# Performance work log

Hardware: AMD Instinct MI355X
Metric: run time of the kernel (lower is better)

## Reference

```python
import jax, jax.numpy as jnp
import numpy as np

N_QUBITS = 12
N_LAYERS = 4
BATCH = 256

# State is kept as shape (batch, 2, 2, ..., 2) with qubit q on axis q+1.
# Z(0) measures the first qubit axis.

def _apply_1q(psi, q, U):
    """Apply a shared 2x2 gate U to qubit q."""
    p = jnp.moveaxis(psi, q + 1, -1)
    p = jnp.einsum('ij,...j->...i', U.astype(psi.dtype), p)
    return jnp.moveaxis(p, -1, q + 1)


def _rz_batch(psi, q, theta):
    """RZ with per-sample angle theta of shape (batch,). RZ = diag(e^{-i t/2}, e^{i t/2})."""
    half = 0.5 * theta
    ph = jnp.stack([jnp.exp(-1j * half), jnp.exp(1j * half)], axis=-1)  # (b, 2)
    ph = ph.reshape((theta.shape[0],) + (1,) * (N_QUBITS - 1) + (2,)).astype(psi.dtype)
    p = jnp.moveaxis(psi, q + 1, -1)
    return jnp.moveaxis(p * ph, -1, q + 1)


def _rz_shared(psi, q, theta):
    """RZ with a scalar (weight) angle shared across the batch."""
    half = 0.5 * theta
    ph = jnp.stack([jnp.exp(-1j * half), jnp.exp(1j * half)]).astype(psi.dtype)  # (2,)
    p = jnp.moveaxis(psi, q + 1, -1)
    return jnp.moveaxis(p * ph, -1, q + 1)


def _ry(psi, q, theta):
    """RY(theta) = [[cos(t/2), -sin(t/2)], [sin(t/2), cos(t/2)]], scalar angle."""
    c, s = jnp.cos(0.5 * theta), jnp.sin(0.5 * theta)
    U = jnp.stack([jnp.stack([c, -s]), jnp.stack([s, c])])
    return _apply_1q(psi, q, U)


def _cx(psi, c, t):
    """CNOT with control c, target t: flip target where control == 1."""
    p = jnp.moveaxis(psi, (c + 1, t + 1), (-2, -1))
    p = jnp.stack([p[..., 0, :], p[..., 1, ::-1]], axis=-2)
    return jnp.moveaxis(p, (-2, -1), (c + 1, t + 1))


def _forward(x, weights):
    b = x.shape[0]
    # H on every qubit starting from |0...0> -> uniform superposition.
    psi = jnp.full((b,) + (2,) * N_QUBITS, np.float32(2.0 ** (-N_QUBITS / 2.0)),
                   dtype=jnp.complex64)
    w = weights.reshape(N_LAYERS, N_QUBITS, 2)  # (layer, qubit, [ry, rz])
    for l in range(N_LAYERS):
        for q in range(N_QUBITS):                 # data re-uploading encoding
            psi = _rz_batch(psi, q, x[:, q])
        for q in range(N_QUBITS):                 # trainable rotations
            psi = _ry(psi, q, w[l, q, 0])
            psi = _rz_shared(psi, q, w[l, q, 1])
        for q in range(N_QUBITS - 1):             # entangling ladder
            psi = _cx(psi, q, q + 1)
    # <Z(0)> = P(qubit0 = 0) - P(qubit0 = 1)
    pr = jnp.sum(jnp.abs(psi) ** 2, axis=tuple(range(2, N_QUBITS + 1)))  # (b, 2)
    return (pr[:, 0] - pr[:, 1])[:, None]  # (b, 1) float32


def setup_inputs() -> dict:
    key = jax.random.key(0)
    kx, kw = jax.random.split(key)
    x = jax.random.normal(kx, (BATCH, N_QUBITS), dtype=jnp.float32)
    weights = jax.random.uniform(kw, (2 * N_LAYERS * N_QUBITS,),
                                 dtype=jnp.float32) * np.float32(2.0 * np.pi)
    return {"x": x, "weights": weights}


def reference(x, weights):
    return _forward(x, weights)
```

## Files before the change

### kernel.cpp

```cpp
#include <hip/hip_runtime.h>

#define NQ 12
#define NL 4
#define DIM 4096
#define BLOCK 512
#define PER_T 8
#define BATCH 256


__device__ __forceinline__ float2 cmul(float2 a, float2 b) {
    return make_float2(a.x * b.x - a.y * b.y, a.x * b.y + a.y * b.x);
}
__device__ __forceinline__ float2 cconj(float2 a) { return make_float2(a.x, -a.y); }

__device__ __forceinline__ float2 fsincos(float ang) {
    float r = ang * 0.15915494309189535f;
    r = r - floorf(r);
    return make_float2(__builtin_amdgcn_cosf(r), __builtin_amdgcn_sinf(r));
}

template <int CTRL>
__device__ __forceinline__ float dppx(float v) {
    int i = __builtin_bit_cast(int, v);
    int r = __builtin_amdgcn_update_dpp(0, i, CTRL, 0xF, 0xF, true);
    return __builtin_bit_cast(float, r);
}
template <int MSK, int CTRL>
__device__ __forceinline__ void ry_dpp(float2* psi, int lane, float c, float s) {
    const float se = (lane & MSK) ? s : -s;
#pragma unroll
    for (int k = 0; k < PER_T; ++k) {
        float px = dppx<CTRL>(psi[k].x);
        float py = dppx<CTRL>(psi[k].y);
        psi[k].x = c * psi[k].x + se * px;
        psi[k].y = c * psi[k].y + se * py;
    }
}
template <int MSK>
__device__ __forceinline__ void ry_shfl(float2* psi, int lane, float c, float s) {
    const float se = (lane & MSK) ? s : -s;
#pragma unroll
    for (int k = 0; k < PER_T; ++k) {
        float px = __shfl_xor(psi[k].x, MSK, 64);
        float py = __shfl_xor(psi[k].y, MSK, 64);
        psi[k].x = c * psi[k].x + se * px;
        psi[k].y = c * psi[k].y + se * py;
    }
}

__global__ __launch_bounds__(BLOCK, 2) void qcp_kernel(
    const float* __restrict__ x,
    const float* __restrict__ w,
    float* __restrict__ out)
{
    __shared__ float2 sP[DIM];
    __shared__ float2 sQ[DIM];
    __shared__ float2 trig[NL * NQ * 2];
    __shared__ float  zhalf[NL * NQ];
    __shared__ float  rbuf[8];

    const int b    = blockIdx.x;
    const int t    = threadIdx.x;
    const int lane = t & 63;
    const int wv   = t >> 6;

    if (t < NL * NQ * 2) trig[t] = fsincos(0.5f * w[t]);
    if (t < NL * NQ) zhalf[t] = 0.5f * w[2 * t + 1];

    float xr[NQ];
#pragma unroll
    for (int q = 0; q < NQ; ++q) xr[q] = x[b * NQ + q];

    int iA[PER_T], iB[PER_T], gI[PER_T];
#pragma unroll
    for (int k = 0; k < PER_T; ++k) {
        iA[k] = lane | (k << 6) | (wv << 9);
        iB[k] = lane | (wv << 6) | (k << 9);
        gI[k] = iA[k] ^ (iA[k] >> 1);
    }

    float2 eph[PER_T];
#pragma unroll
    for (int k = 0; k < PER_T; ++k) {
        int j = iA[k];
        float ang = 0.0f;
#pragma unroll
        for (int q = 0; q < NQ; ++q)
            ang += ((j >> (NQ - 1 - q)) & 1) ? 0.5f * xr[q] : -0.5f * xr[q];
        eph[k] = fsincos(ang);
    }

    float2 psi[PER_T];
#pragma unroll
    for (int k = 0; k < PER_T; ++k) psi[k] = make_float2(0.015625f, 0.0f);

    __syncthreads();

    for (int l = 0; l < NL; ++l) {
        float2 tRY[9];
        float2 tRY0[3], tZ0[3];
        float  zh[6];
        float2 z3, z4, z5;
#pragma unroll
        for (int q = 3; q <= 11; ++q) tRY[q - 3] = trig[(l * NQ + q) * 2];
#pragma unroll
        for (int q = 0; q < 3; ++q) {
            tRY0[q] = trig[(l * NQ + q) * 2 + 0];
            tZ0[q]  = trig[(l * NQ + q) * 2 + 1];
        }
        z3 = trig[(l * NQ + 3) * 2 + 1];
        z4 = trig[(l * NQ + 4) * 2 + 1];
        z5 = trig[(l * NQ + 5) * 2 + 1];
#pragma unroll
        for (int q = 6; q <= 11; ++q) zh[q - 6] = zhalf[l * NQ + q];

#pragma unroll
        for (int k = 0; k < PER_T; ++k) psi[k] = cmul(psi[k], eph[k]);

#pragma unroll
        for (int q = 3; q <= 5; ++q) {
            const int kb = (11 - q) - 6;
            float c = tRY[q - 3].x, s = tRY[q - 3].y;
#pragma unroll
            for (int m = 0; m < PER_T / 2; ++m) {
                int k0 = ((m >> kb) << (kb + 1)) | (m & ((1 << kb) - 1));
                int k1 = k0 | (1 << kb);
                float2 a0 = psi[k0], a1 = psi[k1];
                psi[k0] = make_float2(c * a0.x - s * a1.x, c * a0.y - s * a1.y);
                psi[k1] = make_float2(s * a0.x + c * a1.x, s * a0.y + c * a1.y);
            }
        }

        ry_shfl<32>(psi, lane, tRY[3].x, tRY[3].y);
        ry_shfl<16>(psi, lane, tRY[4].x, tRY[4].y);
        ry_dpp<8, 0x128>(psi, lane, tRY[5].x, tRY[5].y);
        ry_shfl<4>(psi, lane, tRY[6].x, tRY[6].y);
        ry_dpp<2, 0x4E>(psi, lane, tRY[7].x, tRY[7].y);
        ry_dpp<1, 0xB1>(psi, lane, tRY[8].x, tRY[8].y);

        float s_lane = 0.0f;
#pragma unroll
        for (int p = 0; p < 6; ++p)
            s_lane += ((lane >> p) & 1) ? zh[5 - p] : -zh[5 - p];
        {
            float2 base = fsincos(s_lane);
            float2 z45[4];
#pragma unroll
            for (int c2 = 0; c2 < 4; ++c2) {
                float2 a4 = (c2 & 2) ? z4 : cconj(z4);
                float2 a5 = (c2 & 1) ? z5 : cconj(z5);
                z45[c2] = cmul(a4, a5);
            }
#pragma unroll
            for (int k = 0; k < PER_T; ++k) {
                float2 a3 = (k & 4) ? z3 : cconj(z3);
                float2 ph = cmul(cmul(base, a3), z45[k & 3]);
                psi[k] = cmul(psi[k], ph);
            }
        }

#pragma unroll
        for (int k = 0; k < PER_T; ++k) sP[iA[k]] = psi[k];
        __syncthreads();
#pragma unroll
        for (int k = 0; k < PER_T; ++k) psi[k] = sP[iB[k]];

#pragma unroll
        for (int q = 0; q < 3; ++q) {
            const int kb = 2 - q;
            float c = tRY0[q].x, s = tRY0[q].y;
            float2 z = tZ0[q];
#pragma unroll
            for (int m = 0; m < PER_T / 2; ++m) {
                int k0 = ((m >> kb) << (kb + 1)) | (m & ((1 << kb) - 1));
                int k1 = k0 | (1 << kb);
                float2 a0 = psi[k0], a1 = psi[k1];
                float2 n0 = make_float2(c * a0.x - s * a1.x, c * a0.y - s * a1.y);
                float2 n1 = make_float2(s * a0.x + c * a1.x, s * a0.y + c * a1.y);
                psi[k0] = cmul(n0, cconj(z));
                psi[k1] = cmul(n1, z);
            }
        }

#pragma unroll
        for (int k = 0; k < PER_T; ++k) sQ[iB[k]] = psi[k];
        __syncthreads();
#pragma unroll
        for (int k = 0; k < PER_T; ++k) psi[k] = sQ[gI[k]];
    }

    float acc = 0.0f;
#pragma unroll
    for (int k = 0; k < PER_T; ++k)
        acc += psi[k].x * psi[k].x + psi[k].y * psi[k].y;
    if (wv >= 4) acc = -acc;
#pragma unroll
    for (int off = 32; off > 0; off >>= 1)
        acc += __shfl_down(acc, off, 64);
    if (lane == 0) rbuf[wv] = acc;
    __syncthreads();
    if (t == 0) {
        float tot = 0.0f;
#pragma unroll
        for (int i = 0; i < 8; ++i) tot += rbuf[i];
        out[b] = tot;
    }
}

extern "C" void kernel_launch(void* const* d_in, const int* in_sizes, int n_in,
                              void* d_out, int out_size, void* d_ws, size_t ws_size,
                              hipStream_t stream) {
    const float* x = (const float*)d_in[0];
    const float* w = (const float*)d_in[1];
    float* out = (float*)d_out;
    qcp_kernel<<<BATCH, BLOCK, 0, stream>>>(x, w, out);
}
```

Baseline: 70.91 us.

## Fold qubit 6/7 RY+RZ into shared-memory reads, use DPP for xor-4 swap

```diff
diff --git a/kernel.cpp b/kernel.cpp
--- a/kernel.cpp
+++ b/kernel.cpp
@@ -36,13 +36,12 @@
         psi[k].y = c * psi[k].y + se * py;
     }
 }
-template <int MSK>
-__device__ __forceinline__ void ry_shfl(float2* psi, int lane, float c, float s) {
-    const float se = (lane & MSK) ? s : -s;
-#pragma unroll
-    for (int k = 0; k < PER_T; ++k) {
-        float px = __shfl_xor(psi[k].x, MSK, 64);
-        float py = __shfl_xor(psi[k].y, MSK, 64);
+__device__ __forceinline__ void ry_dpp4(float2* psi, int lane, float c, float s) {
+    const float se = (lane & 4) ? s : -s;
+#pragma unroll
+    for (int k = 0; k < PER_T; ++k) {
+        float px = dppx<0x1B>(dppx<0x141>(psi[k].x));
+        float py = dppx<0x1B>(dppx<0x141>(psi[k].y));
         psi[k].x = c * psi[k].x + se * px;
         psi[k].y = c * psi[k].y + se * py;
     }
@@ -99,8 +98,9 @@
     for (int l = 0; l < NL; ++l) {
         float2 tRY[9];
         float2 tRY0[3], tZ0[3];
-        float  zh[6];
+        float  zh[4];
         float2 z3, z4, z5;
+        float2 z6, z7;
 #pragma unroll
         for (int q = 3; q <= 11; ++q) tRY[q - 3] = trig[(l * NQ + q) * 2];
 #pragma unroll
@@ -111,8 +111,10 @@
         z3 = trig[(l * NQ + 3) * 2 + 1];
         z4 = trig[(l * NQ + 4) * 2 + 1];
         z5 = trig[(l * NQ + 5) * 2 + 1];
-#pragma unroll
-        for (int q = 6; q <= 11; ++q) zh[q - 6] = zhalf[l * NQ + q];
+        z6 = trig[(l * NQ + 6) * 2 + 1];
+        z7 = trig[(l * NQ + 7) * 2 + 1];
+#pragma unroll
+        for (int q = 8; q <= 11; ++q) zh[q - 8] = zhalf[l * NQ + q];
 
 #pragma unroll
         for (int k = 0; k < PER_T; ++k) psi[k] = cmul(psi[k], eph[k]);
@@ -131,17 +133,15 @@
             }
         }
 
-        ry_shfl<32>(psi, lane, tRY[3].x, tRY[3].y);
-        ry_shfl<16>(psi, lane, tRY[4].x, tRY[4].y);
         ry_dpp<8, 0x128>(psi, lane, tRY[5].x, tRY[5].y);
-        ry_shfl<4>(psi, lane, tRY[6].x, tRY[6].y);
+        ry_dpp4(psi, lane, tRY[6].x, tRY[6].y);
         ry_dpp<2, 0x4E>(psi, lane, tRY[7].x, tRY[7].y);
         ry_dpp<1, 0xB1>(psi, lane, tRY[8].x, tRY[8].y);
 
         float s_lane = 0.0f;
 #pragma unroll
-        for (int p = 0; p < 6; ++p)
-            s_lane += ((lane >> p) & 1) ? zh[5 - p] : -zh[5 - p];
+        for (int p = 0; p < 4; ++p)
+            s_lane += ((lane >> p) & 1) ? zh[3 - p] : -zh[3 - p];
         {
             float2 base = fsincos(s_lane);
             float2 z45[4];
@@ -161,9 +161,20 @@
 
 #pragma unroll
         for (int k = 0; k < PER_T; ++k) sP[iA[k]] = psi[k];
+
+        const int  b6  = (lane >> 5) & 1;
+        const float c6 = tRY[3].x;
+        const float se6 = b6 ? tRY[3].y : -tRY[3].y;
+        const float2 zb6 = b6 ? z6 : cconj(z6);
         __syncthreads();
 #pragma unroll
-        for (int k = 0; k < PER_T; ++k) psi[k] = sP[iB[k]];
+        for (int k = 0; k < PER_T; ++k) {
+            float2 own = sP[iB[k]];
+            float2 oth = sP[iB[k] ^ 32];
+            float2 n = make_float2(c6 * own.x + se6 * oth.x,
+                                   c6 * own.y + se6 * oth.y);
+            psi[k] = cmul(n, zb6);
+        }
 
 #pragma unroll
         for (int q = 0; q < 3; ++q) {
@@ -184,9 +195,20 @@
 
 #pragma unroll
         for (int k = 0; k < PER_T; ++k) sQ[iB[k]] = psi[k];
+
+        const int  b7  = ((lane >> 4) ^ (lane >> 5)) & 1;
+        const float c7 = tRY[4].x;
+        const float se7 = b7 ? tRY[4].y : -tRY[4].y;
+        const float2 zb7 = b7 ? z7 : cconj(z7);
         __syncthreads();
 #pragma unroll
-        for (int k = 0; k < PER_T; ++k) psi[k] = sQ[gI[k]];
+        for (int k = 0; k < PER_T; ++k) {
+            float2 own = sQ[gI[k]];
+            float2 oth = sQ[gI[k] ^ 16];
+            float2 n = make_float2(c7 * own.x + se7 * oth.x,
+                                   c7 * own.y + se7 * oth.y);
+            psi[k] = cmul(n, zb7);
+        }
     }
 
     float acc = 0.0f;
```

After: 68.88 us. 2.9% less time.
